# Kernel tuning notes

Hardware: AMD Instinct MI355X
Metric: run time of the kernel (lower is better)

Reference implementation:

```python
import jax, jax.numpy as jnp
import numpy as np

D_MODEL = 1024
N_HEAD = 16
SEQ = 2048
BATCH = 2


def setup_inputs() -> dict:
    key = jax.random.key(0)
    x = jax.random.normal(key, (BATCH, SEQ, D_MODEL), dtype=jnp.float32)
    return {"x": x}


def reference(x) -> jnp.ndarray:
    B, S, D = x.shape
    H = N_HEAD
    hd = D // H
    # split heads: q=k=v=x -> [B, H, S, hd]
    qkv = x.reshape(B, S, H, hd).transpose(0, 2, 1, 3)
    q = k = v = qkv
    # scores [B, H, S, S], scaled by sqrt(head_dim)
    w = jnp.einsum("bhqd,bhkd->bhqk", q, k) / jnp.sqrt(jnp.asarray(hd, x.dtype))
    # causal mask (nd == ns == S here)
    causal = jnp.tril(jnp.ones((S, S), dtype=bool))
    mask_value = jnp.finfo(w.dtype).min
    w = jnp.where(causal[None, None, :, :], w, mask_value)
    w = jax.nn.softmax(w, axis=-1)
    out = jnp.einsum("bhqk,bhkd->bhqd", w, v)
    # merge heads -> [B, S, D]
    return out.transpose(0, 2, 1, 3).reshape(B, S, D)
```

## Files before the change

### kernel.cpp

```cpp
#include <hip/hip_runtime.h>

#define BATCH  2
#define SEQ    2048
#define DMODEL 1024
#define NHEAD  16
#define HD     64
#define BH     (BATCH * NHEAD)

typedef __attribute__((ext_vector_type(8))) short s8v;
typedef __attribute__((ext_vector_type(4))) float f4v;

__device__ inline unsigned short bf16_rne(float f) {
    unsigned u = __builtin_bit_cast(unsigned, f);
    u += 0x7FFFu + ((u >> 16) & 1u);
    return (unsigned short)(u >> 16);
}

__global__ __launch_bounds__(256) void prep_kernel(const float* __restrict__ x,
                                                   unsigned short* __restrict__ xb,
                                                   unsigned short* __restrict__ xbT) {
    __shared__ unsigned short tile[64 * 66];
    const int id = blockIdx.x;
    const int bh = id & (BH - 1);
    const int st = id >> 5;
    const int b = bh >> 4, h = bh & (NHEAD - 1);
    const int s0 = st * 64;
    const int tid = threadIdx.x;
    const int c4 = tid & 15, r16 = tid >> 4;

#pragma unroll
    for (int p = 0; p < 4; ++p) {
        const int sl = p * 16 + r16;
        const size_t off = (size_t)(b * SEQ + s0 + sl) * DMODEL + h * HD + c4 * 4;
        float4 v = *(const float4*)(x + off);
        ushort4 o;
        o.x = bf16_rne(v.x); o.y = bf16_rne(v.y);
        o.z = bf16_rne(v.z); o.w = bf16_rne(v.w);
        *(ushort4*)(xb + off) = o;
        unsigned short* t = tile + sl * 66 + c4 * 4;
        t[0] = o.x; t[1] = o.y; t[2] = o.z; t[3] = o.w;
    }
    __syncthreads();
#pragma unroll
    for (int p = 0; p < 4; ++p) {
        const int d = p * 16 + r16;
        ushort4 o;
        o.x = tile[(c4 * 4 + 0) * 66 + d];
        o.y = tile[(c4 * 4 + 1) * 66 + d];
        o.z = tile[(c4 * 4 + 2) * 66 + d];
        o.w = tile[(c4 * 4 + 3) * 66 + d];
        *(ushort4*)(xbT + (size_t)(bh * HD + d) * SEQ + s0 + c4 * 4) = o;
    }
}

__global__ __launch_bounds__(256, 2) void flash_kernel(const unsigned short* __restrict__ xb,
                                                       const unsigned short* __restrict__ xbT,
                                                       float* __restrict__ out) {
    __shared__ __align__(16) char lds[24576];

    const int id = blockIdx.x;
    const int bh = id & (BH - 1);
    const int qt = (SEQ / 64 - 1) - (id >> 5);
    const int b = bh >> 4, h = bh & (NHEAD - 1);
    const int tid = threadIdx.x;
    const int w = tid >> 6;
    const int lane = tid & 63;
    const int n = lane & 15;
    const int g = lane >> 4;
    const int qbase = qt * 64;

    const unsigned short* xbh = xb + (size_t)b * SEQ * DMODEL + h * HD;
    const unsigned short* xTh = xbT + (size_t)bh * HD * SEQ;

    const int qrow = qbase + w * 16 + n;
    const s8v qf0 = *(const s8v*)(xbh + (size_t)qrow * DMODEL + g * 8);
    const s8v qf1 = *(const s8v*)(xbh + (size_t)qrow * DMODEL + 32 + g * 8);

    int roff0[4], roff1[4];
#pragma unroll
    for (int t = 0; t < 4; ++t) {
        roff0[t] = (t * 16 + n) * 128 + ((g ^ (n & 7)) * 16);
        roff1[t] = (t * 16 + n) * 128 + (((4 + g) ^ (n & 7)) * 16);
    }

    f4v o0 = {0.f, 0.f, 0.f, 0.f}, o1 = o0, o2 = o0, o3 = o0, l4 = o0;
    char* const Pbase = lds + 16384 + w * 2048;

    const int sr = lane >> 3;
    const int sc = lane & 7;

    for (int kt = 0; kt <= qt; ++kt) {
        const int k0 = kt * 64;
        __syncthreads();
        if (w < 2) {
#pragma unroll
            for (int i = 0; i < 4; ++i) {
                const int r = w * 32 + i * 8 + sr;
                const unsigned short* gsrc =
                    xbh + (size_t)(k0 + r) * DMODEL + ((sc ^ (r & 7)) * 8);
                const int loff = __builtin_amdgcn_readfirstlane((w * 32 + i * 8) * 128);
                __builtin_amdgcn_global_load_lds(
                    (const __attribute__((address_space(1))) void*)gsrc,
                    (__attribute__((address_space(3))) void*)(lds + loff), 16, 0, 0);
            }
        } else {
#pragma unroll
            for (int i = 0; i < 4; ++i) {
                const int d = (w - 2) * 32 + i * 8 + sr;
                const unsigned short* gsrc =
                    xTh + (size_t)d * SEQ + k0 + ((sc ^ (d & 7)) * 8);
                const int loff =
                    __builtin_amdgcn_readfirstlane(8192 + ((w - 2) * 32 + i * 8) * 128);
                __builtin_amdgcn_global_load_lds(
                    (const __attribute__((address_space(1))) void*)gsrc,
                    (__attribute__((address_space(3))) void*)(lds + loff), 16, 0, 0);
            }
        }
        __syncthreads();

        const bool diag = (kt == qt);
#pragma unroll
        for (int t = 0; t < 4; ++t) {
            const s8v kb0 = *(const s8v*)(lds + roff0[t]);
            const s8v kb1 = *(const s8v*)(lds + roff1[t]);
            f4v c = {0.f, 0.f, 0.f, 0.f};
            c = __builtin_amdgcn_mfma_f32_16x16x32_bf16(qf0, kb0, c, 0, 0, 0);
            c = __builtin_amdgcn_mfma_f32_16x16x32_bf16(qf1, kb1, c, 0, 0, 0);
#pragma unroll
            for (int r = 0; r < 4; ++r) {
                float p = __builtin_amdgcn_exp2f(c[r] * 0.18033688011112042f);
                if (diag)
                    p = ((t * 16 + n) <= (w * 16 + g * 4 + r)) ? p : 0.0f;
                l4[r] += p;
                const int Lp = (g * 4 + r) | ((((t * 2) + (n >> 3)) & 3) << 4);
                *(unsigned short*)(Pbase + (t >> 1) * 1024 + Lp * 16 + (n & 7) * 2) =
                    bf16_rne(p);
            }
        }

        const s8v pa0 = *(const s8v*)(Pbase + lane * 16);
        const s8v pa1 = *(const s8v*)(Pbase + 1024 + lane * 16);
        const char* kColB = lds + 8192;
        {
            s8v vb;
            vb = *(const s8v*)(kColB + roff0[0]);
            o0 = __builtin_amdgcn_mfma_f32_16x16x32_bf16(pa0, vb, o0, 0, 0, 0);
            vb = *(const s8v*)(kColB + roff1[0]);
            o0 = __builtin_amdgcn_mfma_f32_16x16x32_bf16(pa1, vb, o0, 0, 0, 0);
            vb = *(const s8v*)(kColB + roff0[1]);
            o1 = __builtin_amdgcn_mfma_f32_16x16x32_bf16(pa0, vb, o1, 0, 0, 0);
            vb = *(const s8v*)(kColB + roff1[1]);
            o1 = __builtin_amdgcn_mfma_f32_16x16x32_bf16(pa1, vb, o1, 0, 0, 0);
            vb = *(const s8v*)(kColB + roff0[2]);
            o2 = __builtin_amdgcn_mfma_f32_16x16x32_bf16(pa0, vb, o2, 0, 0, 0);
            vb = *(const s8v*)(kColB + roff1[2]);
            o2 = __builtin_amdgcn_mfma_f32_16x16x32_bf16(pa1, vb, o2, 0, 0, 0);
            vb = *(const s8v*)(kColB + roff0[3]);
            o3 = __builtin_amdgcn_mfma_f32_16x16x32_bf16(pa0, vb, o3, 0, 0, 0);
            vb = *(const s8v*)(kColB + roff1[3]);
            o3 = __builtin_amdgcn_mfma_f32_16x16x32_bf16(pa1, vb, o3, 0, 0, 0);
        }
    }

#pragma unroll
    for (int m = 1; m < 16; m <<= 1) {
        l4[0] += __shfl_xor(l4[0], m, 64);
        l4[1] += __shfl_xor(l4[1], m, 64);
        l4[2] += __shfl_xor(l4[2], m, 64);
        l4[3] += __shfl_xor(l4[3], m, 64);
    }
    f4v inv;
    inv[0] = 1.0f / l4[0];
    inv[1] = 1.0f / l4[1];
    inv[2] = 1.0f / l4[2];
    inv[3] = 1.0f / l4[3];

    float* outh = out + (size_t)b * SEQ * DMODEL + h * HD;
#pragma unroll
    for (int r = 0; r < 4; ++r) {
        const size_t rowoff = (size_t)(qbase + w * 16 + g * 4 + r) * DMODEL;
        outh[rowoff + 0 * 16 + n] = o0[r] * inv[r];
        outh[rowoff + 1 * 16 + n] = o1[r] * inv[r];
        outh[rowoff + 2 * 16 + n] = o2[r] * inv[r];
        outh[rowoff + 3 * 16 + n] = o3[r] * inv[r];
    }
}

#define KT 32
#define QR 16
#define LDS_STRIDE 68

__global__ __launch_bounds__(64, 2)
void attn_fp32_kernel(const float* __restrict__ x, float* __restrict__ out) {
    __shared__ float kv[KT * LDS_STRIDE];
    const int id = blockIdx.x;
    const int bh = id & (BATCH * NHEAD - 1);
    const int qt = (SEQ / QR - 1) - (id >> 5);
    const int b = bh >> 4, h = bh & (NHEAD - 1);
    const int lane = threadIdx.x;
    const int row = lane & (QR - 1);
    const int slice = lane >> 4;
    const int qrow = qt * QR + row;
    const float* xh = x + (size_t)b * SEQ * DMODEL + (size_t)h * HD;
    float q[HD], o[HD];
    const float4* qp = (const float4*)(xh + (size_t)qrow * DMODEL);
#pragma unroll
    for (int i = 0; i < HD / 4; ++i) {
        float4 v = qp[i];
        q[4*i+0] = v.x * 0.125f; q[4*i+1] = v.y * 0.125f;
        q[4*i+2] = v.z * 0.125f; q[4*i+3] = v.w * 0.125f;
    }
#pragma unroll
    for (int d = 0; d < HD; ++d) o[d] = 0.0f;
    float l = 0.0f;
    const int kend = qt * QR + QR;
    for (int kt0 = 0; kt0 < kend; kt0 += KT) {
        __syncthreads();
#pragma unroll
        for (int i = 0; i < (KT * HD / 4) / 64; ++i) {
            int idx = i * 64 + lane;
            int r = idx >> 4, c = idx & 15;
            *(float4*)(kv + r * LDS_STRIDE + c * 4) =
                *(const float4*)(xh + (size_t)(kt0 + r) * DMODEL + c * 4);
        }
        __syncthreads();
#pragma unroll 2
        for (int jj = 0; jj < KT / 4; ++jj) {
            const int j = jj * 4 + slice;
            const float* kr = kv + j * LDS_STRIDE;
            float a0 = 0.f, a1 = 0.f, a2 = 0.f, a3 = 0.f;
#pragma unroll
            for (int dq = 0; dq < 16; ++dq) {
                float4 kk = ((const float4*)kr)[dq];
                a0 = fmaf(q[4*dq+0], kk.x, a0); a1 = fmaf(q[4*dq+1], kk.y, a1);
                a2 = fmaf(q[4*dq+2], kk.z, a2); a3 = fmaf(q[4*dq+3], kk.w, a3);
            }
            float p = __expf((a0 + a1) + (a2 + a3));
            p = (kt0 + j <= qrow) ? p : 0.0f;
            l += p;
#pragma unroll
            for (int dq = 0; dq < 16; ++dq) {
                float4 vv = ((const float4*)kr)[dq];
                o[4*dq+0] = fmaf(p, vv.x, o[4*dq+0]); o[4*dq+1] = fmaf(p, vv.y, o[4*dq+1]);
                o[4*dq+2] = fmaf(p, vv.z, o[4*dq+2]); o[4*dq+3] = fmaf(p, vv.w, o[4*dq+3]);
            }
        }
    }
    l += __shfl_xor(l, 16, 64);
    l += __shfl_xor(l, 32, 64);
#pragma unroll
    for (int d = 0; d < HD; ++d) {
        o[d] += __shfl_xor(o[d], 16, 64);
        o[d] += __shfl_xor(o[d], 32, 64);
    }
    if (slice == 0) {
        const float invl = 1.0f / l;
        float4* op = (float4*)(out + ((size_t)b * SEQ + qrow) * DMODEL + (size_t)h * HD);
#pragma unroll
        for (int i = 0; i < HD / 4; ++i) {
            float4 v;
            v.x = o[4*i+0] * invl; v.y = o[4*i+1] * invl;
            v.z = o[4*i+2] * invl; v.w = o[4*i+3] * invl;
            op[i] = v;
        }
    }
}

extern "C" void kernel_launch(void* const* d_in, const int* in_sizes, int n_in,
                              void* d_out, int out_size, void* d_ws, size_t ws_size,
                              hipStream_t stream) {
    const float* x = (const float*)d_in[0];
    float* out = (float*)d_out;
    const size_t need = (size_t)2 * BATCH * SEQ * DMODEL * 2;
    if (ws_size >= need) {
        unsigned short* xb  = (unsigned short*)d_ws;
        unsigned short* xbT = xb + (size_t)BATCH * SEQ * DMODEL;
        hipLaunchKernelGGL(prep_kernel, dim3(BH * SEQ / 64), dim3(256), 0, stream, x, xb, xbT);
        hipLaunchKernelGGL(flash_kernel, dim3(BH * SEQ / 64), dim3(256), 0, stream, xb, xbT, out);
    } else {
        hipLaunchKernelGGL(attn_fp32_kernel, dim3(BATCH * NHEAD * (SEQ / QR)), dim3(64), 0,
                           stream, x, out);
    }
}
```

Before: 113.5 us.

## Double-buffer K/V tiles with async prefetch, raise occupancy, rebalance tile order

The key/value tile loads move into a helper that writes into one of two LDS buffers. The next tile is now prefetched with async global-to-LDS loads while the current tile is computed, which removes one barrier per iteration and hides load latency behind the MFMA work. LDS grows to 40 KB, and the launch bound rises from 2 to 4 blocks per CU. Query tiles are issued in an interleaved heavy/light order to balance the causal work across CUs. s_setprio brackets around the MFMA groups favour the matrix work. The risks are register pressure under the tighter launch bound, and correctness depends on the barrier waiting for the outstanding LDS-DMA loads.

```diff
diff --git a/kernel.cpp b/kernel.cpp
--- a/kernel.cpp
+++ b/kernel.cpp
@@ -53,14 +53,47 @@
     }
 }
 
-__global__ __launch_bounds__(256, 2) void flash_kernel(const unsigned short* __restrict__ xb,
+__device__ __forceinline__ void stage_tile(const unsigned short* __restrict__ xbh,
+                                           const unsigned short* __restrict__ xTh,
+                                           char* lds, int bufoff, int k0,
+                                           int w, int sr, int sc) {
+    if (w < 2) {
+#pragma unroll
+        for (int i = 0; i < 4; ++i) {
+            const int r = w * 32 + i * 8 + sr;
+            const unsigned short* gsrc =
+                xbh + (size_t)(k0 + r) * DMODEL + ((sc ^ (r & 7)) * 8);
+            const int loff = __builtin_amdgcn_readfirstlane(bufoff + (w * 32 + i * 8) * 128);
+            __builtin_amdgcn_global_load_lds(
+                (const __attribute__((address_space(1))) void*)gsrc,
+                (__attribute__((address_space(3))) void*)(lds + loff), 16, 0, 0);
+        }
+    } else {
+#pragma unroll
+        for (int i = 0; i < 4; ++i) {
+            const int d = (w - 2) * 32 + i * 8 + sr;
+            const unsigned short* gsrc =
+                xTh + (size_t)d * SEQ + k0 + ((sc ^ (d & 7)) * 8);
+            const int loff =
+                __builtin_amdgcn_readfirstlane(bufoff + 8192 + ((w - 2) * 32 + i * 8) * 128);
+            __builtin_amdgcn_global_load_lds(
+                (const __attribute__((address_space(1))) void*)gsrc,
+                (__attribute__((address_space(3))) void*)(lds + loff), 16, 0, 0);
+        }
+    }
+}
+
+__global__ __launch_bounds__(256, 4) void flash_kernel(const unsigned short* __restrict__ xb,
                                                        const unsigned short* __restrict__ xbT,
                                                        float* __restrict__ out) {
-    __shared__ __align__(16) char lds[24576];
+    __shared__ __align__(16) char lds[40960];
 
     const int id = blockIdx.x;
     const int bh = id & (BH - 1);
-    const int qt = (SEQ / 64 - 1) - (id >> 5);
+    const int t5 = id >> 5;
+    const int rr = t5 >> 3, uu = t5 & 7;
+    const int qt = (rr == 0) ? (31 - uu) : (rr == 1) ? (16 + uu)
+                 : (rr == 2) ? (15 - uu) : uu;
     const int b = bh >> 4, h = bh & (NHEAD - 1);
     const int tid = threadIdx.x;
     const int w = tid >> 6;
@@ -84,48 +117,29 @@
     }
 
     f4v o0 = {0.f, 0.f, 0.f, 0.f}, o1 = o0, o2 = o0, o3 = o0, l4 = o0;
-    char* const Pbase = lds + 16384 + w * 2048;
+    char* const Pbase = lds + 32768 + w * 2048;
 
     const int sr = lane >> 3;
     const int sc = lane & 7;
 
+    stage_tile(xbh, xTh, lds, 0, 0, w, sr, sc);
+
     for (int kt = 0; kt <= qt; ++kt) {
-        const int k0 = kt * 64;
+        char* const buf = lds + ((kt & 1) << 14);
         __syncthreads();
-        if (w < 2) {
-#pragma unroll
-            for (int i = 0; i < 4; ++i) {
-                const int r = w * 32 + i * 8 + sr;
-                const unsigned short* gsrc =
-                    xbh + (size_t)(k0 + r) * DMODEL + ((sc ^ (r & 7)) * 8);
-                const int loff = __builtin_amdgcn_readfirstlane((w * 32 + i * 8) * 128);
-                __builtin_amdgcn_global_load_lds(
-                    (const __attribute__((address_space(1))) void*)gsrc,
-                    (__attribute__((address_space(3))) void*)(lds + loff), 16, 0, 0);
-            }
-        } else {
-#pragma unroll
-            for (int i = 0; i < 4; ++i) {
-                const int d = (w - 2) * 32 + i * 8 + sr;
-                const unsigned short* gsrc =
-                    xTh + (size_t)d * SEQ + k0 + ((sc ^ (d & 7)) * 8);
-                const int loff =
-                    __builtin_amdgcn_readfirstlane(8192 + ((w - 2) * 32 + i * 8) * 128);
-                __builtin_amdgcn_global_load_lds(
-                    (const __attribute__((address_space(1))) void*)gsrc,
-                    (__attribute__((address_space(3))) void*)(lds + loff), 16, 0, 0);
-            }
-        }
-        __syncthreads();
+        if (kt < qt)
+            stage_tile(xbh, xTh, lds, ((kt & 1) ^ 1) << 14, (kt + 1) * 64, w, sr, sc);
 
         const bool diag = (kt == qt);
 #pragma unroll
         for (int t = 0; t < 4; ++t) {
-            const s8v kb0 = *(const s8v*)(lds + roff0[t]);
-            const s8v kb1 = *(const s8v*)(lds + roff1[t]);
+            const s8v kb0 = *(const s8v*)(buf + roff0[t]);
+            const s8v kb1 = *(const s8v*)(buf + roff1[t]);
             f4v c = {0.f, 0.f, 0.f, 0.f};
+            __builtin_amdgcn_s_setprio(1);
             c = __builtin_amdgcn_mfma_f32_16x16x32_bf16(qf0, kb0, c, 0, 0, 0);
             c = __builtin_amdgcn_mfma_f32_16x16x32_bf16(qf1, kb1, c, 0, 0, 0);
+            __builtin_amdgcn_s_setprio(0);
 #pragma unroll
             for (int r = 0; r < 4; ++r) {
                 float p = __builtin_amdgcn_exp2f(c[r] * 0.18033688011112042f);
@@ -140,9 +154,10 @@
 
         const s8v pa0 = *(const s8v*)(Pbase + lane * 16);
         const s8v pa1 = *(const s8v*)(Pbase + 1024 + lane * 16);
-        const char* kColB = lds + 8192;
+        const char* kColB = buf + 8192;
         {
             s8v vb;
+            __builtin_amdgcn_s_setprio(1);
             vb = *(const s8v*)(kColB + roff0[0]);
             o0 = __builtin_amdgcn_mfma_f32_16x16x32_bf16(pa0, vb, o0, 0, 0, 0);
             vb = *(const s8v*)(kColB + roff1[0]);
@@ -159,6 +174,7 @@
             o3 = __builtin_amdgcn_mfma_f32_16x16x32_bf16(pa0, vb, o3, 0, 0, 0);
             vb = *(const s8v*)(kColB + roff1[3]);
             o3 = __builtin_amdgcn_mfma_f32_16x16x32_bf16(pa1, vb, o3, 0, 0, 0);
+            __builtin_amdgcn_s_setprio(0);
         }
     }
 
```

Result: faster. 105.6 us (-7.0%).
